# Optimization experiments

Hardware: AMD Instinct MI355X
Metric: run time of the kernel (lower is better)

The kernel has to match this reference:

```python
import jax, jax.numpy as jnp
import numpy as np

TEMPERATURE = 0.07


def sparsemax(z):
    """Sparsemax along the last axis (Martins & Astudillo, 2016)."""
    n = z.shape[-1]
    z_sorted = -jnp.sort(-z, axis=-1)                      # descending sort
    k = jnp.arange(1, n + 1, dtype=z.dtype)
    cum = jnp.cumsum(z_sorted, axis=-1)
    support = (1.0 + k * z_sorted) > cum                   # support set indicator
    k_z = jnp.sum(support, axis=-1, keepdims=True)         # support size per row
    idx = k_z.astype(jnp.int32) - 1
    cum_kz = jnp.take_along_axis(cum, idx, axis=-1)
    tau = (cum_kz - 1.0) / k_z.astype(z.dtype)             # threshold
    return jnp.maximum(z - tau, 0.0)


def setup_inputs() -> dict:
    key = jax.random.key(0)
    k1, k2 = jax.random.split(key)
    B, V, D = 2048, 2, 128
    features = jax.random.normal(k1, (B, V, D), dtype=jnp.float32)
    attention_scores = jax.random.normal(k2, (V * B, V * B), dtype=jnp.float32)
    return {"features": features, "attention_scores": attention_scores}


def reference(features, attention_scores):
    B, V, D = features.shape
    N = V * B
    dt = features.dtype

    # default mask path (labels=None, mask=None): identity over the batch
    mask = jnp.eye(B, dtype=dt)

    # L2-normalize features along feature dim, flatten views (row-major, as torch .view)
    f = features / jnp.linalg.norm(features, axis=-1, keepdims=True)
    f = f.reshape(N, D)

    # cosine similarities / temperature, row-max subtracted (detached)
    sim = jnp.matmul(f, f.T) / TEMPERATURE                  # [N, N]
    sim = sim - jax.lax.stop_gradient(jnp.max(sim, axis=-1, keepdims=True))

    big_mask = jnp.tile(mask, (V, V))                       # mask.repeat(V, V)
    eye_n = jnp.eye(N, dtype=dt)
    positive_mask = big_mask - eye_n
    negative_mask = 1.0 - big_mask

    masked_scores = sparsemax((attention_scores * negative_mask) / TEMPERATURE)

    exp_sim = jnp.exp(sim) * (positive_mask + negative_mask - masked_scores)
    log_prob = sim - jnp.log(jnp.sum(exp_sim, axis=-1, keepdims=True))

    mean_log_prob_pos = jnp.sum(log_prob * positive_mask, axis=1) / jnp.sum(positive_mask, axis=1)
    loss = -jnp.mean(mean_log_prob_pos)                     # reduction='mean'
    return loss, masked_scores
```

## Files before the change

### kernel.cpp

```cpp
#include <hip/hip_runtime.h>
#include <math.h>

#define NN   4096
#define BD   2048
#define DF   128
#define INV_T (1.0f/0.07f)
#define SUPP_CAP 32

typedef __attribute__((ext_vector_type(8))) short short8v;
typedef __attribute__((ext_vector_type(4))) float float4v;

__device__ inline unsigned short f2bf_rne(float x) {
  unsigned int u = __float_as_uint(x);
  u = (u + 0x7FFFu + ((u >> 16) & 1u)) >> 16;
  return (unsigned short)u;
}
__device__ inline float bf2f(unsigned short h) {
  return __uint_as_float(((unsigned int)h) << 16);
}

__global__ void k_prep(const float* __restrict__ feat,
                       unsigned short* __restrict__ fbf,
                       float* __restrict__ Zv) {
  int gid  = blockIdx.x * blockDim.x + threadIdx.x;
  int row  = gid >> 6;
  int lane = threadIdx.x & 63;
  const float2* src = (const float2*)(feat + (size_t)row * DF);
  float2 v = src[lane];
  float ss = v.x * v.x + v.y * v.y;
  #pragma unroll
  for (int off = 1; off < 64; off <<= 1) ss += __shfl_xor(ss, off, 64);
  float inv = rsqrtf(ss);
  ushort2 o;
  o.x = f2bf_rne(v.x * inv);
  o.y = f2bf_rne(v.y * inv);
  ((ushort2*)(fbf + (size_t)row * DF))[lane] = o;
  if (gid < NN) Zv[gid] = 0.f;
}

__global__ __launch_bounds__(256) void k_sparsemax(
    const float* __restrict__ attn,
    float* __restrict__ msOut,
    int* __restrict__ suppCnt,
    int* __restrict__ suppIdx,
    float* __restrict__ suppVal) {
  __shared__ float redS[4], redC[4];
  __shared__ int scnt;
  int row  = blockIdx.x;
  int tid  = threadIdx.x;
  int lane = tid & 63, wv = tid >> 6;
  const float4* arow = (const float4*)(attn + (size_t)row * NN);
  int rb = row & (BD - 1);
  float z[16];
  #pragma unroll
  for (int u = 0; u < 4; ++u) {
    int q = u * 256 + tid;
    float4 a = arow[q];
    int j = q * 4;
    z[4*u+0] = (((j+0) & (BD-1)) == rb) ? 0.f : a.x * INV_T;
    z[4*u+1] = (((j+1) & (BD-1)) == rb) ? 0.f : a.y * INV_T;
    z[4*u+2] = (((j+2) & (BD-1)) == rb) ? 0.f : a.z * INV_T;
    z[4*u+3] = (((j+3) & (BD-1)) == rb) ? 0.f : a.w * INV_T;
  }
  float m = z[0];
  #pragma unroll
  for (int u = 1; u < 16; ++u) m = fmaxf(m, z[u]);
  #pragma unroll
  for (int off = 1; off < 64; off <<= 1) m = fmaxf(m, __shfl_xor(m, off, 64));
  if (lane == 0) redS[wv] = m;
  __syncthreads();
  m = fmaxf(fmaxf(redS[0], redS[1]), fmaxf(redS[2], redS[3]));

  float tau = m - 1.0f;
  #pragma unroll 1
  for (int it = 0; it < 8; ++it) {
    float S = 0.f, C = 0.f;
    #pragma unroll
    for (int u = 0; u < 16; ++u) {
      bool in = z[u] > tau;
      S += in ? z[u] : 0.f;
      C += in ? 1.f : 0.f;
    }
    #pragma unroll
    for (int off = 1; off < 64; off <<= 1) {
      S += __shfl_xor(S, off, 64);
      C += __shfl_xor(C, off, 64);
    }
    __syncthreads();
    if (lane == 0) { redS[wv] = S; redC[wv] = C; }
    __syncthreads();
    S = (redS[0] + redS[1]) + (redS[2] + redS[3]);
    C = (redC[0] + redC[1]) + (redC[2] + redC[3]);
    tau = (C > 0.f) ? (S - 1.0f) / C : tau;
  }
  if (tid == 0) scnt = 0;
  __syncthreads();

  float* orow = msOut + (size_t)row * NN;
  #pragma unroll
  for (int u = 0; u < 4; ++u) {
    int j = (u * 256 + tid) * 4;
    #pragma unroll
    for (int t = 0; t < 4; ++t) {
      float msv = fmaxf(z[4*u+t] - tau, 0.f);
      orow[j+t] = msv;
      if (msv > 0.f) {
        int slot = atomicAdd(&scnt, 1);
        if (slot < SUPP_CAP) {
          suppIdx[row * SUPP_CAP + slot] = j + t;
          suppVal[row * SUPP_CAP + slot] = msv;
        }
      }
    }
  }
  __syncthreads();
  if (tid == 0) suppCnt[row] = min(scnt, SUPP_CAP);
}

__global__ __launch_bounds__(256) void k_gram(
    const unsigned short* __restrict__ fbf, float* __restrict__ Zv) {
  int tid = threadIdx.x;
  int wave = tid >> 6, lane = tid & 63;
  int c = lane & 15, quad = lane >> 4;
  int wi = wave >> 1, wj = wave & 1;
  int i0 = blockIdx.y * 128 + wi * 64;
  int j0 = blockIdx.x * 128 + wj * 64;

  const unsigned short* aBase = fbf + (size_t)(i0 + c) * DF + quad * 8;
  const unsigned short* bBase = fbf + (size_t)(j0 + c) * DF + quad * 8;

  float4v acc[4][4];
  #pragma unroll
  for (int m = 0; m < 4; ++m)
    #pragma unroll
    for (int n = 0; n < 4; ++n) acc[m][n] = (float4v){0.f, 0.f, 0.f, 0.f};

  #pragma unroll
  for (int k0 = 0; k0 < DF; k0 += 32) {
    short8v afr[4], bfr[4];
    #pragma unroll
    for (int m = 0; m < 4; ++m)
      afr[m] = *(const short8v*)(aBase + (size_t)(m * 16) * DF + k0);
    #pragma unroll
    for (int n = 0; n < 4; ++n)
      bfr[n] = *(const short8v*)(bBase + (size_t)(n * 16) * DF + k0);
    #pragma unroll
    for (int m = 0; m < 4; ++m)
      #pragma unroll
      for (int n = 0; n < 4; ++n)
        acc[m][n] = __builtin_amdgcn_mfma_f32_16x16x32_bf16(
            afr[m], bfr[n], acc[m][n], 0, 0, 0);
  }

  #pragma unroll
  for (int m = 0; m < 4; ++m) {
    #pragma unroll
    for (int r = 0; r < 4; ++r) {
      int i = i0 + m * 16 + quad * 4 + r;
      float zsum = 0.f;
      #pragma unroll
      for (int n = 0; n < 4; ++n) {
        int j = j0 + n * 16 + c;
        float e = __expf(acc[m][n][r] * INV_T - INV_T);
        zsum += (i == j) ? 0.f : e;
      }
      zsum += __shfl_xor(zsum, 1, 64);
      zsum += __shfl_xor(zsum, 2, 64);
      zsum += __shfl_xor(zsum, 4, 64);
      zsum += __shfl_xor(zsum, 8, 64);
      if (c == 0) atomicAdd(&Zv[i], zsum);
    }
  }
}

__global__ __launch_bounds__(256) void k_corr(
    const unsigned short* __restrict__ fbf,
    const int* __restrict__ suppCnt, const int* __restrict__ suppIdx,
    const float* __restrict__ suppVal,
    float* __restrict__ Zv, float* __restrict__ numer) {
  int tid = threadIdx.x;
  int wave = tid >> 6, lane = tid & 63;
  int row = blockIdx.x * 4 + wave;
  ushort2 a = ((const ushort2*)(fbf + (size_t)row * DF))[lane];
  float ax = bf2f(a.x), ay = bf2f(a.y);

  int pos = (row + BD) & (NN - 1);
  ushort2 b = ((const ushort2*)(fbf + (size_t)pos * DF))[lane];
  float d = ax * bf2f(b.x) + ay * bf2f(b.y);
  #pragma unroll
  for (int off = 1; off < 64; off <<= 1) d += __shfl_xor(d, off, 64);
  if (lane == 0) numer[row] = d * INV_T - INV_T;

  int cnt = suppCnt[row];
  float corr = 0.f;
  for (int e = 0; e < cnt; ++e) {
    int j = suppIdx[row * SUPP_CAP + e];
    float v = suppVal[row * SUPP_CAP + e];
    ushort2 g = ((const ushort2*)(fbf + (size_t)j * DF))[lane];
    float s = ax * bf2f(g.x) + ay * bf2f(g.y);
    #pragma unroll
    for (int off = 1; off < 64; off <<= 1) s += __shfl_xor(s, off, 64);
    corr += __expf(s * INV_T - INV_T) * v;
  }
  if (lane == 0 && cnt > 0) atomicAdd(&Zv[row], -corr);
}

__global__ void k_loss(const float* __restrict__ Zv,
                       const float* __restrict__ numer,
                       float* __restrict__ out) {
  float acc = 0.f;
  for (int i = threadIdx.x; i < NN; i += 256)
    acc += numer[i] - logf(Zv[i]);
  #pragma unroll
  for (int off = 1; off < 64; off <<= 1) acc += __shfl_xor(acc, off, 64);
  __shared__ float red[4];
  int wv = threadIdx.x >> 6, lane = threadIdx.x & 63;
  if (lane == 0) red[wv] = acc;
  __syncthreads();
  if (threadIdx.x == 0) {
    float t = (red[0] + red[1]) + (red[2] + red[3]);
    out[0] = -t / (float)NN;
  }
}

extern "C" void kernel_launch(void* const* d_in, const int* in_sizes, int n_in,
                              void* d_out, int out_size, void* d_ws, size_t ws_size,
                              hipStream_t stream) {
  const float* feat = (const float*)d_in[0];
  const float* attn = (const float*)d_in[1];
  float* out = (float*)d_out;
  float* msOut = out + 1;

  float* Zv       = (float*)d_ws;
  float* numer    = Zv + NN;
  int*   suppCnt  = (int*)(numer + NN);
  int*   suppIdx  = suppCnt + NN;
  float* suppVal  = (float*)(suppIdx + (size_t)NN * SUPP_CAP);
  unsigned short* fbf = (unsigned short*)(suppVal + (size_t)NN * SUPP_CAP);

  k_prep<<<dim3(1024), dim3(256), 0, stream>>>(feat, fbf, Zv);
  k_sparsemax<<<dim3(4096), dim3(256), 0, stream>>>(attn, msOut, suppCnt,
                                                    suppIdx, suppVal);
  k_gram<<<dim3(32, 32), dim3(256), 0, stream>>>(fbf, Zv);
  k_corr<<<dim3(1024), dim3(256), 0, stream>>>(fbf, suppCnt, suppIdx, suppVal,
                                               Zv, numer);
  k_loss<<<dim3(1), dim3(256), 0, stream>>>(Zv, numer, out);
}
```

Before: 178.4 us.

## Solve sparsemax threshold on a shared candidate list and fold positive logit into gram

The sparsemax kernel now collects only the entries within 1 of the row max into shared memory. A single thread then iterates the threshold fixed point to convergence on that short list. This replaces eight block-wide reduction passes over all 4096 values, each with two barriers. The output row is written as 4-wide vectors, with the support scatter done only for nonzero groups. The positive-pair logit is captured inside the gram kernel's epilogue, so the correction kernel no longer loads the partner row and can exit early for rows with empty support. In exchange, the threshold solve runs serially on one thread, and the candidate list is capped at 128 entries.

```diff
diff --git a/kernel.cpp b/kernel.cpp
--- a/kernel.cpp
+++ b/kernel.cpp
@@ -6,9 +6,11 @@
 #define DF   128
 #define INV_T (1.0f/0.07f)
 #define SUPP_CAP 32
+#define CAND_CAP 128
 
 typedef __attribute__((ext_vector_type(8))) short short8v;
 typedef __attribute__((ext_vector_type(4))) float float4v;
+typedef float f4a __attribute__((ext_vector_type(4), aligned(4)));
 
 __device__ inline unsigned short f2bf_rne(float x) {
   unsigned int u = __float_as_uint(x);
@@ -44,8 +46,10 @@
     int* __restrict__ suppCnt,
     int* __restrict__ suppIdx,
     float* __restrict__ suppVal) {
-  __shared__ float redS[4], redC[4];
-  __shared__ int scnt;
+  __shared__ float redM[4];
+  __shared__ float cand[CAND_CAP];
+  __shared__ int ccnt;
+  __shared__ float tauS;
   int row  = blockIdx.x;
   int tid  = threadIdx.x;
   int lane = tid & 63, wv = tid >> 6;
@@ -67,48 +71,69 @@
   for (int u = 1; u < 16; ++u) m = fmaxf(m, z[u]);
   #pragma unroll
   for (int off = 1; off < 64; off <<= 1) m = fmaxf(m, __shfl_xor(m, off, 64));
-  if (lane == 0) redS[wv] = m;
-  __syncthreads();
-  m = fmaxf(fmaxf(redS[0], redS[1]), fmaxf(redS[2], redS[3]));
-
-  float tau = m - 1.0f;
-  #pragma unroll 1
-  for (int it = 0; it < 8; ++it) {
-    float S = 0.f, C = 0.f;
-    #pragma unroll
-    for (int u = 0; u < 16; ++u) {
-      bool in = z[u] > tau;
-      S += in ? z[u] : 0.f;
-      C += in ? 1.f : 0.f;
-    }
-    #pragma unroll
-    for (int off = 1; off < 64; off <<= 1) {
-      S += __shfl_xor(S, off, 64);
-      C += __shfl_xor(C, off, 64);
-    }
-    __syncthreads();
-    if (lane == 0) { redS[wv] = S; redC[wv] = C; }
-    __syncthreads();
-    S = (redS[0] + redS[1]) + (redS[2] + redS[3]);
-    C = (redC[0] + redC[1]) + (redC[2] + redC[3]);
-    tau = (C > 0.f) ? (S - 1.0f) / C : tau;
-  }
+  if (lane == 0) redM[wv] = m;
+  if (tid == 0) ccnt = 0;
+  __syncthreads();
+  m = fmaxf(fmaxf(redM[0], redM[1]), fmaxf(redM[2], redM[3]));
+
+  float thresh = m - 1.0f;
+  #pragma unroll
+  for (int u = 0; u < 16; ++u) {
+    if (z[u] > thresh) {
+      int slot = atomicAdd(&ccnt, 1);
+      if (slot < CAND_CAP) cand[slot] = z[u];
+    }
+  }
+  __syncthreads();
+
+  if (tid == 0) {
+    int nc = min(ccnt, CAND_CAP);
+    float tau = thresh;
+    #pragma unroll 1
+    for (int it = 0; it < 32; ++it) {
+      float S = 0.f; float C = 0.f;
+      for (int e = 0; e < nc; ++e) {
+        float v = cand[e];
+        if (v > tau) { S += v; C += 1.f; }
+      }
+      float nt = (C > 0.f) ? (S - 1.0f) / C : tau;
+      if (nt == tau) break;
+      tau = nt;
+    }
+    tauS = tau;
+  }
+  __syncthreads();
+  float tau = tauS;
+  if (tid == 0) {
+    int sc = 0;
+    int nc = min(ccnt, CAND_CAP);
+    (void)nc;
+    suppCnt[row] = 0;
+  }
+
+  float* orow = msOut + (size_t)row * NN;
+  __shared__ int scnt;
   if (tid == 0) scnt = 0;
   __syncthreads();
-
-  float* orow = msOut + (size_t)row * NN;
   #pragma unroll
   for (int u = 0; u < 4; ++u) {
     int j = (u * 256 + tid) * 4;
-    #pragma unroll
-    for (int t = 0; t < 4; ++t) {
-      float msv = fmaxf(z[4*u+t] - tau, 0.f);
-      orow[j+t] = msv;
-      if (msv > 0.f) {
-        int slot = atomicAdd(&scnt, 1);
-        if (slot < SUPP_CAP) {
-          suppIdx[row * SUPP_CAP + slot] = j + t;
-          suppVal[row * SUPP_CAP + slot] = msv;
+    f4a v;
+    v.x = fmaxf(z[4*u+0] - tau, 0.f);
+    v.y = fmaxf(z[4*u+1] - tau, 0.f);
+    v.z = fmaxf(z[4*u+2] - tau, 0.f);
+    v.w = fmaxf(z[4*u+3] - tau, 0.f);
+    *((f4a*)(orow + j)) = v;
+    if (v.x > 0.f || v.y > 0.f || v.z > 0.f || v.w > 0.f) {
+      float mv[4] = {v.x, v.y, v.z, v.w};
+      #pragma unroll
+      for (int t = 0; t < 4; ++t) {
+        if (mv[t] > 0.f) {
+          int slot = atomicAdd(&scnt, 1);
+          if (slot < SUPP_CAP) {
+            suppIdx[row * SUPP_CAP + slot] = j + t;
+            suppVal[row * SUPP_CAP + slot] = mv[t];
+          }
         }
       }
     }
@@ -118,7 +143,8 @@
 }
 
 __global__ __launch_bounds__(256) void k_gram(
-    const unsigned short* __restrict__ fbf, float* __restrict__ Zv) {
+    const unsigned short* __restrict__ fbf, float* __restrict__ Zv,
+    float* __restrict__ numer) {
   int tid = threadIdx.x;
   int wave = tid >> 6, lane = tid & 63;
   int c = lane & 15, quad = lane >> 4;
@@ -157,12 +183,15 @@
     #pragma unroll
     for (int r = 0; r < 4; ++r) {
       int i = i0 + m * 16 + quad * 4 + r;
+      int pos = (i + BD) & (NN - 1);
       float zsum = 0.f;
       #pragma unroll
       for (int n = 0; n < 4; ++n) {
         int j = j0 + n * 16 + c;
-        float e = __expf(acc[m][n][r] * INV_T - INV_T);
+        float simv = acc[m][n][r] * INV_T - INV_T;
+        float e = __expf(simv);
         zsum += (i == j) ? 0.f : e;
+        if (j == pos) numer[i] = simv;
       }
       zsum += __shfl_xor(zsum, 1, 64);
       zsum += __shfl_xor(zsum, 2, 64);
@@ -176,22 +205,14 @@
 __global__ __launch_bounds__(256) void k_corr(
     const unsigned short* __restrict__ fbf,
     const int* __restrict__ suppCnt, const int* __restrict__ suppIdx,
-    const float* __restrict__ suppVal,
-    float* __restrict__ Zv, float* __restrict__ numer) {
+    const float* __restrict__ suppVal, float* __restrict__ Zv) {
   int tid = threadIdx.x;
   int wave = tid >> 6, lane = tid & 63;
   int row = blockIdx.x * 4 + wave;
+  int cnt = suppCnt[row];
+  if (cnt == 0) return;
   ushort2 a = ((const ushort2*)(fbf + (size_t)row * DF))[lane];
   float ax = bf2f(a.x), ay = bf2f(a.y);
-
-  int pos = (row + BD) & (NN - 1);
-  ushort2 b = ((const ushort2*)(fbf + (size_t)pos * DF))[lane];
-  float d = ax * bf2f(b.x) + ay * bf2f(b.y);
-  #pragma unroll
-  for (int off = 1; off < 64; off <<= 1) d += __shfl_xor(d, off, 64);
-  if (lane == 0) numer[row] = d * INV_T - INV_T;
-
-  int cnt = suppCnt[row];
   float corr = 0.f;
   for (int e = 0; e < cnt; ++e) {
     int j = suppIdx[row * SUPP_CAP + e];
@@ -202,7 +223,7 @@
     for (int off = 1; off < 64; off <<= 1) s += __shfl_xor(s, off, 64);
     corr += __expf(s * INV_T - INV_T) * v;
   }
-  if (lane == 0 && cnt > 0) atomicAdd(&Zv[row], -corr);
+  if (lane == 0) atomicAdd(&Zv[row], -corr);
 }
 
 __global__ void k_loss(const float* __restrict__ Zv,
@@ -241,8 +262,7 @@
   k_prep<<<dim3(1024), dim3(256), 0, stream>>>(feat, fbf, Zv);
   k_sparsemax<<<dim3(4096), dim3(256), 0, stream>>>(attn, msOut, suppCnt,
                                                     suppIdx, suppVal);
-  k_gram<<<dim3(32, 32), dim3(256), 0, stream>>>(fbf, Zv);
-  k_corr<<<dim3(1024), dim3(256), 0, stream>>>(fbf, suppCnt, suppIdx, suppVal,
-                                               Zv, numer);
+  k_gram<<<dim3(32, 32), dim3(256), 0, stream>>>(fbf, Zv, numer);
+  k_corr<<<dim3(1024), dim3(256), 0, stream>>>(fbf, suppCnt, suppIdx, suppVal, Zv);
   k_loss<<<dim3(1), dim3(256), 0, stream>>>(Zv, numer, out);
 }
```

Measured after the change: 160.2 us. -10.2%, faster.
